# Performance work log

Hardware: AMD Instinct MI355X
Metric: run time of the kernel (lower is better)

The kernel has to match this reference:

```python
import jax, jax.numpy as jnp
import numpy as np

A, N, D, H, L, V = 2048, 64, 256, 8, 2, 119
DH = D // H


def _ln(x, g, b, eps=1e-5):
    m = x.mean(-1, keepdims=True)
    v = ((x - m) ** 2).mean(-1, keepdims=True)
    return (x - m) * jax.lax.rsqrt(v + eps) * g + b


def setup_inputs() -> dict:
    key = jax.random.key(0)
    ks = iter(jax.random.split(key, 64))
    nk = lambda: next(ks)
    inp = {
        'species': jax.random.randint(nk(), (A,), 0, V),
        'neighbor_species': jax.random.randint(nk(), (A, N), 0, V),
        'edge_vectors': jax.random.normal(nk(), (A, N, 3), jnp.float32),
        'edge_distances': jax.random.uniform(nk(), (A, N), jnp.float32) * 4.5,
        'padding_mask': jnp.zeros((A, N), bool),
        'reverse_neighbor_index': jax.random.randint(nk(), (A * N,), 0, A * N),
        'cutoff_factors': jax.random.uniform(nk(), (A, N), jnp.float32),
    }
    s = 0.05
    p = {
        'node_embed': jax.random.normal(nk(), (L, V, D), jnp.float32) * s,
        'neigh_embed': jax.random.normal(nk(), (V, D), jnp.float32) * s,
        'W_edge': jax.random.normal(nk(), (L, 4, D), jnp.float32) * s,
        'b_edge': jnp.zeros((L, D), jnp.float32),
        'ln1_g': jnp.ones((L, D), jnp.float32), 'ln1_b': jnp.zeros((L, D), jnp.float32),
        'Wqkv': jax.random.normal(nk(), (L, D, 3 * D), jnp.float32) * s,
        'bqkv': jnp.zeros((L, 3 * D), jnp.float32),
        'Wo': jax.random.normal(nk(), (L, D, D), jnp.float32) * s,
        'bo': jnp.zeros((L, D), jnp.float32),
        'ln2_g': jnp.ones((L, D), jnp.float32), 'ln2_b': jnp.zeros((L, D), jnp.float32),
        'Wff1': jax.random.normal(nk(), (L, D, 4 * D), jnp.float32) * s,
        'bff1': jnp.zeros((L, 4 * D), jnp.float32),
        'Wff2': jax.random.normal(nk(), (L, 4 * D, D), jnp.float32) * s,
        'bff2': jnp.zeros((L, D), jnp.float32),
        'Wnode': jax.random.normal(nk(), (L, D, D), jnp.float32) * s,
        'bnode': jnp.zeros((L, D), jnp.float32),
        'Wnh': jax.random.normal(nk(), (L, D, D), jnp.float32) * s,
        'bnh': jnp.zeros((L, D), jnp.float32),
        'Wnf': jax.random.normal(nk(), (L, D, 1), jnp.float32) * s,
        'bnf': jnp.zeros((L, 1), jnp.float32),
        'Weh': jax.random.normal(nk(), (L, D, D), jnp.float32) * s,
        'beh': jnp.zeros((L, D), jnp.float32),
        'Wef': jax.random.normal(nk(), (L, D, 1), jnp.float32) * s,
        'bef': jnp.zeros((L, 1), jnp.float32),
    }
    inp.update(p)
    return inp


def reference(species, neighbor_species, edge_vectors, edge_distances, padding_mask,
              reverse_neighbor_index, cutoff_factors, node_embed, neigh_embed,
              W_edge, b_edge, ln1_g, ln1_b, Wqkv, bqkv, Wo, bo, ln2_g, ln2_b,
              Wff1, bff1, Wff2, bff2, Wnode, bnode, Wnh, bnh, Wnf, bnf,
              Weh, beh, Wef, bef):
    inv = 1.0 / jnp.sqrt(jnp.asarray(DH, edge_vectors.dtype))
    mask = padding_mask  # [A,N] True = padded
    valid = (~mask).astype(edge_vectors.dtype)
    msgs = neigh_embed[neighbor_species]  # [A,N,D] gather (irregular)
    energies = jnp.zeros((A,), edge_vectors.dtype)
    for l in range(L):
        nodes = node_embed[l][species]  # [A,D]
        efeat = jnp.concatenate([edge_vectors, edge_distances[..., None]], -1)  # [A,N,4]
        eemb = jax.nn.gelu(efeat @ W_edge[l] + b_edge[l])
        x = msgs + eemb + nodes[:, None, :]  # [A,N,D] tokens
        # --- neighbor attention, modulated by cutoff envelope ---
        h = _ln(x, ln1_g[l], ln1_b[l])
        qkv = h @ Wqkv[l] + bqkv[l]
        q, k, v = jnp.split(qkv, 3, axis=-1)
        q = q.reshape(A, N, H, DH); k = k.reshape(A, N, H, DH); v = v.reshape(A, N, H, DH)
        scores = jnp.einsum('aihd,ajhd->ahij', q, k) * inv  # [A,H,N,N]
        scores = jnp.where(mask[:, None, None, :], -1e9, scores)
        probs = jax.nn.softmax(scores, axis=-1) * cutoff_factors[:, None, None, :]
        attn = jnp.einsum('ahij,ajhd->aihd', probs, v).reshape(A, N, D)
        x = x + attn @ Wo[l] + bo[l]
        h2 = _ln(x, ln2_g[l], ln2_b[l])
        x = x + jax.nn.gelu(h2 @ Wff1[l] + bff1[l]) @ Wff2[l] + bff2[l]
        output_edge = jnp.where(mask[..., None], 0.0, x)  # [A,N,D]
        pooled = (output_edge * (cutoff_factors * valid)[..., None]).sum(1)
        output_node = nodes + pooled @ Wnode[l] + bnode[l]
        # --- per-layer energy heads ---
        node_e = jax.nn.gelu(output_node @ Wnh[l] + bnh[l]) @ Wnf[l] + bnf[l]  # [A,1]
        edge_e = jax.nn.gelu(output_edge @ Weh[l] + beh[l]) @ Wef[l] + bef[l]  # [A,N,1]
        edge_e = jnp.where(mask[..., None], 0.0, edge_e)
        energies = energies + node_e[:, 0] + (edge_e[..., 0] * cutoff_factors).sum(1)
        # --- reverse-message scatter/gather mixing ---
        rev = output_edge.reshape(A * N, D)[reverse_neighbor_index].reshape(A, N, D)
        rev = jnp.where(mask[..., None], 0.0, rev)
        msgs = 0.5 * (msgs + rev)
    return energies
```

## Files before the change

### kernel.cpp

```cpp
#include <hip/hip_runtime.h>
#include <cstdint>


constexpr int A_ = 2048, N_ = 64, D_ = 256, H_ = 8, L_ = 2, V_ = 119;
constexpr int AN_ = A_ * N_;

typedef unsigned short bf16;
typedef __attribute__((ext_vector_type(4))) unsigned short u16x4;
typedef __attribute__((ext_vector_type(8))) short s16x8;
typedef __attribute__((ext_vector_type(4))) float f32x4;

__device__ __forceinline__ float bf2f(bf16 u) { return __uint_as_float((unsigned)u << 16); }
__device__ __forceinline__ bf16 f2bf(float f) {
  unsigned u = __float_as_uint(f);
  return (bf16)((u + 0x7fffu + ((u >> 16) & 1u)) >> 16);
}
__device__ __forceinline__ float4 ld4(const float* p) { return *(const float4*)p; }
__device__ __forceinline__ float4 ld4(const bf16* p) {
  u16x4 u = *(const u16x4*)p;
  return make_float4(bf2f(u.x), bf2f(u.y), bf2f(u.z), bf2f(u.w));
}
__device__ __forceinline__ void st4(float* p, float4 v) { *(float4*)p = v; }
__device__ __forceinline__ void st4(bf16* p, float4 v) {
  u16x4 u;
  u.x = f2bf(v.x); u.y = f2bf(v.y); u.z = f2bf(v.z); u.w = f2bf(v.w);
  *(u16x4*)p = u;
}
__device__ __forceinline__ float lds1(const float* p) { return *p; }
__device__ __forceinline__ float lds1(const bf16* p) { return bf2f(*p); }
__device__ __forceinline__ void sts1(float* p, float v) { *p = v; }
__device__ __forceinline__ void sts1(bf16* p, float v) { *p = f2bf(v); }

__device__ __forceinline__ float gelu_f(float x) {
  float z2 = 1.5957691216057308f * x * (1.f + 0.044715f * x * x);
  float e = __expf(-z2);
  return x * __builtin_amdgcn_rcpf(1.f + e);
}

__device__ __forceinline__ float wave_sum(float s) {
#pragma unroll
  for (int off = 32; off > 0; off >>= 1) s += __shfl_down(s, off, 64);
  return __shfl(s, 0, 64);
}

__device__ __forceinline__ void gload_lds16(const bf16* g, void* lds) {
  __builtin_amdgcn_global_load_lds(
      (const __attribute__((address_space(1))) unsigned int*)g,
      (__attribute__((address_space(3))) unsigned int*)lds, 16, 0, 0);
}

__global__ void zero_kernel(float* p, int n) {
  int i = blockIdx.x * 256 + threadIdx.x;
  if (i < n) p[i] = 0.f;
}

__global__ __launch_bounds__(256) void wt_kernel(
    const float* __restrict__ W, bf16* __restrict__ Wt, int K, int N) {
  int idx = blockIdx.x * 256 + threadIdx.x;
  if (idx >= K * N) return;
  int k = idx / N, n = idx - k * N;
  Wt[(size_t)n * K + k] = f2bf(W[idx]);
}

__global__ __launch_bounds__(256) void init_msgs_kernel(
    const int* __restrict__ ns, const float* __restrict__ ne, bf16* __restrict__ msgs) {
  int t = blockIdx.x, d = threadIdx.x;
  msgs[(size_t)t * D_ + d] = f2bf(ne[(size_t)ns[t] * D_ + d]);
}

__global__ __launch_bounds__(256) void gather_nodes_kernel(
    const int* __restrict__ species, const float* __restrict__ node_embed_l,
    float* __restrict__ nodesbuf) {
  int a = blockIdx.x, d = threadIdx.x;
  nodesbuf[(size_t)a * D_ + d] = node_embed_l[(size_t)species[a] * D_ + d];
}

__global__ __launch_bounds__(256) void build_x_ln_kernel(
    const bf16* __restrict__ msgs, const float* __restrict__ ev,
    const float* __restrict__ ed, const float* __restrict__ We,
    const float* __restrict__ be, const float* __restrict__ nodesbuf,
    const float* __restrict__ lng, const float* __restrict__ lnb,
    bf16* __restrict__ x, bf16* __restrict__ h, int token0) {
  int lt = blockIdx.x * 4 + (threadIdx.x >> 6);
  int t = token0 + lt;
  int lane = threadIdx.x & 63;
  int d4 = lane << 2;
  int a = t >> 6;
  float e0 = ev[(size_t)t * 3 + 0];
  float e1 = ev[(size_t)t * 3 + 1];
  float e2 = ev[(size_t)t * 3 + 2];
  float dd = ed[t];
  float4 m = ld4(msgs + (size_t)t * D_ + d4);
  float4 nb = ld4(nodesbuf + (size_t)a * D_ + d4);
  float4 w0 = ld4(We + d4);
  float4 w1 = ld4(We + D_ + d4);
  float4 w2 = ld4(We + 2 * D_ + d4);
  float4 w3 = ld4(We + 3 * D_ + d4);
  float4 bb = ld4(be + d4);
  float r[4];
  {
    float mm[4] = {m.x, m.y, m.z, m.w};
    float nn[4] = {nb.x, nb.y, nb.z, nb.w};
    float ww0[4] = {w0.x, w0.y, w0.z, w0.w};
    float ww1[4] = {w1.x, w1.y, w1.z, w1.w};
    float ww2[4] = {w2.x, w2.y, w2.z, w2.w};
    float ww3[4] = {w3.x, w3.y, w3.z, w3.w};
    float bbv[4] = {bb.x, bb.y, bb.z, bb.w};
#pragma unroll
    for (int c = 0; c < 4; ++c) {
      float tt = e0 * ww0[c] + e1 * ww1[c] + e2 * ww2[c] + dd * ww3[c] + bbv[c];
      r[c] = mm[c] + gelu_f(tt) + nn[c];
    }
  }
  st4(x + (size_t)lt * D_ + d4, make_float4(r[0], r[1], r[2], r[3]));
  float s = wave_sum(r[0] + r[1] + r[2] + r[3]);
  float mean = s * (1.f / 256.f);
  float c0 = r[0] - mean, c1 = r[1] - mean, c2 = r[2] - mean, c3 = r[3] - mean;
  float q = wave_sum(c0 * c0 + c1 * c1 + c2 * c2 + c3 * c3);
  float rstd = rsqrtf(q * (1.f / 256.f) + 1e-5f);
  float4 g4 = *(const float4*)(lng + d4);
  float4 b4 = *(const float4*)(lnb + d4);
  float4 o;
  o.x = c0 * rstd * g4.x + b4.x;
  o.y = c1 * rstd * g4.y + b4.y;
  o.z = c2 * rstd * g4.z + b4.z;
  o.w = c3 * rstd * g4.w + b4.w;
  st4(h + (size_t)lt * D_ + d4, o);
}

__global__ __launch_bounds__(256) void ln_apply_kernel(
    const bf16* __restrict__ x, const float* __restrict__ gw,
    const float* __restrict__ bw, bf16* __restrict__ h) {
  int row = blockIdx.x * 4 + (threadIdx.x >> 6);
  int lane = threadIdx.x & 63;
  float4 v = ld4(x + (size_t)row * D_ + lane * 4);
  float s = wave_sum(v.x + v.y + v.z + v.w);
  float mean = s * (1.f / 256.f);
  float dx = v.x - mean, dy = v.y - mean, dz = v.z - mean, dw = v.w - mean;
  float q = wave_sum(dx * dx + dy * dy + dz * dz + dw * dw);
  float rstd = rsqrtf(q * (1.f / 256.f) + 1e-5f);
  float4 g4 = *(const float4*)(gw + lane * 4);
  float4 b4 = *(const float4*)(bw + lane * 4);
  float4 o;
  o.x = dx * rstd * g4.x + b4.x;
  o.y = dy * rstd * g4.y + b4.y;
  o.z = dz * rstd * g4.z + b4.z;
  o.w = dw * rstd * g4.w + b4.w;
  st4(h + (size_t)row * D_ + lane * 4, o);
}

template <bool GELU, bool RES, typename TC>
__global__ __launch_bounds__(256) void mfma_gemm_kernel(
    const bf16* __restrict__ A, const bf16* __restrict__ Bt,
    const float* __restrict__ bias, const TC* __restrict__ Rp, TC* __restrict__ Cp,
    int M, int N, int K) {
  __shared__ __align__(16) char AlsB[128 * 64];
  __shared__ __align__(16) char BlsB[128 * 64];
  const int nb = N >> 7;
  const int bx = blockIdx.x % nb;
  const int by = blockIdx.x / nb;
  const int tid = threadIdx.x;
  const int w = tid >> 6, l = tid & 63;
  const int wm = w >> 1, wn = w & 1;
  const int srow = l >> 2;
  const int kg = (l & 3) ^ ((l >> 3) & 3);
  const bf16* Ag = A + (size_t)(by * 128 + w * 32 + srow) * K + kg * 8;
  const bf16* Bg = Bt + (size_t)(bx * 128 + w * 32 + srow) * K + kg * 8;
  char* AlsW = AlsB + w * 2048;
  char* BlsW = BlsB + w * 2048;
  const int frow = l & 15;
  const int soff = (((l >> 4) ^ ((l >> 1) & 3)) << 4);
  const char* Ar = AlsB + (wm * 64 + frow) * 64 + soff;
  const char* Br = BlsB + (wn * 64 + frow) * 64 + soff;

  f32x4 acc[4][4] = {};
  for (int k0 = 0; k0 < K; k0 += 32) {
    __syncthreads();
    gload_lds16(Ag + k0, AlsW);
    gload_lds16(Ag + (size_t)16 * K + k0, AlsW + 1024);
    gload_lds16(Bg + k0, BlsW);
    gload_lds16(Bg + (size_t)16 * K + k0, BlsW + 1024);
    __syncthreads();
    s16x8 af[4], bfr[4];
#pragma unroll
    for (int mi = 0; mi < 4; ++mi) af[mi] = *(const s16x8*)(Ar + mi * 1024);
#pragma unroll
    for (int nj = 0; nj < 4; ++nj) bfr[nj] = *(const s16x8*)(Br + nj * 1024);
#pragma unroll
    for (int mi = 0; mi < 4; ++mi)
#pragma unroll
      for (int nj = 0; nj < 4; ++nj)
        acc[mi][nj] = __builtin_amdgcn_mfma_f32_16x16x32_bf16(af[mi], bfr[nj],
                                                              acc[mi][nj], 0, 0, 0);
  }
  const int r0 = (l >> 4) << 2;
#pragma unroll
  for (int mi = 0; mi < 4; ++mi) {
    int rowb = by * 128 + wm * 64 + mi * 16 + r0;
#pragma unroll
    for (int r = 0; r < 4; ++r) {
      size_t rowoff = (size_t)(rowb + r) * N;
#pragma unroll
      for (int nj = 0; nj < 4; ++nj) {
        int col = bx * 128 + wn * 64 + nj * 16 + frow;
        float v = acc[mi][nj][r] + bias[col];
        if constexpr (GELU) v = gelu_f(v);
        if constexpr (RES) v += lds1(Rp + rowoff + col);
        sts1(Cp + rowoff + col, v);
      }
    }
  }
}

__global__ __launch_bounds__(256) void edge_head_kernel(
    const bf16* __restrict__ A, const bf16* __restrict__ Bt,
    const float* __restrict__ bias, const float* __restrict__ wef,
    float* __restrict__ edge_e, int M, int N, int K) {
  __shared__ __align__(16) char AlsB[128 * 64];
  __shared__ __align__(16) char BlsB[128 * 64];
  const int nb = N >> 7;
  const int bx = blockIdx.x % nb;
  const int by = blockIdx.x / nb;
  const int tid = threadIdx.x;
  const int w = tid >> 6, l = tid & 63;
  const int wm = w >> 1, wn = w & 1;
  const int srow = l >> 2;
  const int kg = (l & 3) ^ ((l >> 3) & 3);
  const bf16* Ag = A + (size_t)(by * 128 + w * 32 + srow) * K + kg * 8;
  const bf16* Bg = Bt + (size_t)(bx * 128 + w * 32 + srow) * K + kg * 8;
  char* AlsW = AlsB + w * 2048;
  char* BlsW = BlsB + w * 2048;
  const int frow = l & 15;
  const int soff = (((l >> 4) ^ ((l >> 1) & 3)) << 4);
  const char* Ar = AlsB + (wm * 64 + frow) * 64 + soff;
  const char* Br = BlsB + (wn * 64 + frow) * 64 + soff;

  f32x4 acc[4][4] = {};
  for (int k0 = 0; k0 < K; k0 += 32) {
    __syncthreads();
    gload_lds16(Ag + k0, AlsW);
    gload_lds16(Ag + (size_t)16 * K + k0, AlsW + 1024);
    gload_lds16(Bg + k0, BlsW);
    gload_lds16(Bg + (size_t)16 * K + k0, BlsW + 1024);
    __syncthreads();
    s16x8 af[4], bfr[4];
#pragma unroll
    for (int mi = 0; mi < 4; ++mi) af[mi] = *(const s16x8*)(Ar + mi * 1024);
#pragma unroll
    for (int nj = 0; nj < 4; ++nj) bfr[nj] = *(const s16x8*)(Br + nj * 1024);
#pragma unroll
    for (int mi = 0; mi < 4; ++mi)
#pragma unroll
      for (int nj = 0; nj < 4; ++nj)
        acc[mi][nj] = __builtin_amdgcn_mfma_f32_16x16x32_bf16(af[mi], bfr[nj],
                                                              acc[mi][nj], 0, 0, 0);
  }
  const int r0 = (l >> 4) << 2;
#pragma unroll
  for (int mi = 0; mi < 4; ++mi) {
#pragma unroll
    for (int r = 0; r < 4; ++r) {
      float s = 0.f;
#pragma unroll
      for (int nj = 0; nj < 4; ++nj) {
        int col = bx * 128 + wn * 64 + nj * 16 + frow;
        s += gelu_f(acc[mi][nj][r] + bias[col]) * wef[col];
      }
      s += __shfl_xor(s, 1, 64);
      s += __shfl_xor(s, 2, 64);
      s += __shfl_xor(s, 4, 64);
      s += __shfl_xor(s, 8, 64);
      if (frow == 0) {
        int row = by * 128 + wm * 64 + mi * 16 + r0 + r;
        atomicAdd(&edge_e[row], s);
      }
    }
  }
}

template <bool GELU, bool RES>
__global__ __launch_bounds__(256) void vgemm_kernel(
    const float* __restrict__ Ap, const float* __restrict__ Bp,
    const float* __restrict__ bias, const float* __restrict__ Rp,
    float* __restrict__ Cp, int M, int N, int K) {
  __shared__ float As[16][65];
  __shared__ float Bs[16][65];
  int nb = N >> 6;
  int bx = blockIdx.x % nb;
  int by = blockIdx.x / nb;
  int tid = threadIdx.x;
  int tx = tid & 15, ty = tid >> 4;
  int am = tid >> 2, akq = (tid & 3) << 2;
  int bk = tid >> 4, bc = (tid & 15) << 2;
  const float* Ab = Ap + (size_t)(by * 64) * K;
  const float* Bb = Bp + bx * 64;
  float acc[4][4] = {};
  for (int k0 = 0; k0 < K; k0 += 16) {
    float4 av = ld4(Ab + (size_t)am * K + k0 + akq);
    As[akq + 0][am] = av.x; As[akq + 1][am] = av.y;
    As[akq + 2][am] = av.z; As[akq + 3][am] = av.w;
    float4 bv4 = ld4(Bb + (size_t)(k0 + bk) * N + bc);
    Bs[bk][bc + 0] = bv4.x; Bs[bk][bc + 1] = bv4.y;
    Bs[bk][bc + 2] = bv4.z; Bs[bk][bc + 3] = bv4.w;
    __syncthreads();
#pragma unroll
    for (int k = 0; k < 16; ++k) {
      float ar[4], br[4];
#pragma unroll
      for (int i = 0; i < 4; ++i) ar[i] = As[k][ty * 4 + i];
#pragma unroll
      for (int j = 0; j < 4; ++j) br[j] = Bs[k][tx * 4 + j];
#pragma unroll
      for (int i = 0; i < 4; ++i)
#pragma unroll
        for (int j = 0; j < 4; ++j) acc[i][j] += ar[i] * br[j];
    }
    __syncthreads();
  }
#pragma unroll
  for (int i = 0; i < 4; ++i) {
    int row = by * 64 + ty * 4 + i;
    int col0 = bx * 64 + tx * 4;
    float4 v = make_float4(acc[i][0], acc[i][1], acc[i][2], acc[i][3]);
    float4 bs = *(const float4*)(bias + col0);
    v.x += bs.x; v.y += bs.y; v.z += bs.z; v.w += bs.w;
    if constexpr (GELU) {
      v.x = gelu_f(v.x); v.y = gelu_f(v.y); v.z = gelu_f(v.z); v.w = gelu_f(v.w);
    }
    if constexpr (RES) {
      float4 r = ld4(Rp + (size_t)row * N + col0);
      v.x += r.x; v.y += r.y; v.z += r.z; v.w += r.w;
    }
    st4(Cp + (size_t)row * N + col0, v);
  }
}

__global__ __launch_bounds__(64) void attn_kernel(
    const bf16* __restrict__ qkv, const float* __restrict__ cutoff,
    const unsigned char* __restrict__ mask, bf16* __restrict__ out, int atom0) {
  int al = blockIdx.x >> 3;
  int h = blockIdx.x & 7;
  int a = atom0 + al;
  int lane = threadIdx.x;
  __shared__ __align__(16) char Pl[64 * 128];
  __shared__ __align__(16) char Vt[32 * 128];
  const bf16* base = qkv + (size_t)al * (64 * 768);
  const int fr = lane & 15;
  const int kg8 = (lane >> 4) << 3;
  const int r0 = (lane >> 4) << 2;
  s16x8 qf[4], kf[4];
#pragma unroll
  for (int mi = 0; mi < 4; ++mi)
    qf[mi] = *(const s16x8*)(base + (size_t)(mi * 16 + fr) * 768 + h * 32 + kg8);
#pragma unroll
  for (int nj = 0; nj < 4; ++nj)
    kf[nj] = *(const s16x8*)(base + (size_t)(nj * 16 + fr) * 768 + 256 + h * 32 + kg8);
  {
    int vrow = lane >> 3;
    int d4 = (lane & 7) << 2;
#pragma unroll
    for (int it = 0; it < 8; ++it) {
      int row = it * 8 + vrow;
      u16x4 v = *(const u16x4*)(base + (size_t)row * 768 + 512 + h * 32 + d4);
#pragma unroll
      for (int c = 0; c < 4; ++c) {
        int d = d4 + c;
        int byt = (d * 128 + row * 2) ^ ((d & 7) << 4);
        *(bf16*)(Vt + byt) = v[c];
      }
    }
  }
  f32x4 s[4][4];
#pragma unroll
  for (int mi = 0; mi < 4; ++mi)
#pragma unroll
    for (int nj = 0; nj < 4; ++nj) {
      f32x4 z = {0.f, 0.f, 0.f, 0.f};
      s[mi][nj] = __builtin_amdgcn_mfma_f32_16x16x32_bf16(qf[mi], kf[nj], z, 0, 0, 0);
    }
  const float inv = 0.17677669529663687f;
  float cwj[4], mskj[4];
#pragma unroll
  for (int nj = 0; nj < 4; ++nj) {
    int j = nj * 16 + fr;
    cwj[nj] = cutoff[(size_t)a * 64 + j];
    mskj[nj] = mask[(size_t)a * 64 + j] ? 1.f : 0.f;
  }
  float rden[4][4];
#pragma unroll
  for (int mi = 0; mi < 4; ++mi) {
    float rm[4] = {-3e38f, -3e38f, -3e38f, -3e38f};
#pragma unroll
    for (int nj = 0; nj < 4; ++nj)
#pragma unroll
      for (int r = 0; r < 4; ++r) {
        float v = s[mi][nj][r] * inv;
        if (mskj[nj] != 0.f) v = -1e9f;
        s[mi][nj][r] = v;
        rm[r] = fmaxf(rm[r], v);
      }
#pragma unroll
    for (int r = 0; r < 4; ++r) {
      rm[r] = fmaxf(rm[r], __shfl_xor(rm[r], 1, 64));
      rm[r] = fmaxf(rm[r], __shfl_xor(rm[r], 2, 64));
      rm[r] = fmaxf(rm[r], __shfl_xor(rm[r], 4, 64));
      rm[r] = fmaxf(rm[r], __shfl_xor(rm[r], 8, 64));
    }
    float dn[4] = {0.f, 0.f, 0.f, 0.f};
#pragma unroll
    for (int nj = 0; nj < 4; ++nj)
#pragma unroll
      for (int r = 0; r < 4; ++r) {
        float e = __expf(s[mi][nj][r] - rm[r]);
        s[mi][nj][r] = e;
        dn[r] += e;
      }
#pragma unroll
    for (int r = 0; r < 4; ++r) {
      dn[r] += __shfl_xor(dn[r], 1, 64);
      dn[r] += __shfl_xor(dn[r], 2, 64);
      dn[r] += __shfl_xor(dn[r], 4, 64);
      dn[r] += __shfl_xor(dn[r], 8, 64);
      rden[mi][r] = dn[r];
    }
#pragma unroll
    for (int nj = 0; nj < 4; ++nj)
#pragma unroll
      for (int r = 0; r < 4; ++r) {
        int row = mi * 16 + r0 + r;
        int byt = (row * 128 + (nj * 16 + fr) * 2) ^ ((row & 7) << 4);
        *(bf16*)(Pl + byt) = f2bf(s[mi][nj][r] * cwj[nj]);
      }
  }
  __syncthreads();
  s16x8 bfv[2][2];
#pragma unroll
  for (int dj = 0; dj < 2; ++dj)
#pragma unroll
    for (int kk = 0; kk < 2; ++kk) {
      int d = dj * 16 + fr;
      int byt = (d * 128 + (kk * 32 + kg8) * 2) ^ ((d & 7) << 4);
      bfv[dj][kk] = *(const s16x8*)(Vt + byt);
    }
  f32x4 o[4][2] = {};
#pragma unroll
  for (int mi = 0; mi < 4; ++mi) {
#pragma unroll
    for (int kk = 0; kk < 2; ++kk) {
      int row = mi * 16 + fr;
      int byt = (row * 128 + (kk * 32 + kg8) * 2) ^ ((row & 7) << 4);
      s16x8 af = *(const s16x8*)(Pl + byt);
#pragma unroll
      for (int dj = 0; dj < 2; ++dj)
        o[mi][dj] = __builtin_amdgcn_mfma_f32_16x16x32_bf16(af, bfv[dj][kk],
                                                            o[mi][dj], 0, 0, 0);
    }
  }
#pragma unroll
  for (int mi = 0; mi < 4; ++mi) {
#pragma unroll
    for (int r = 0; r < 4; ++r) {
      float scr = __builtin_amdgcn_rcpf(rden[mi][r]);
      int row = mi * 16 + r0 + r;
      bf16* orow = out + (size_t)(al * 64 + row) * D_ + h * 32;
#pragma unroll
      for (int dj = 0; dj < 2; ++dj)
        orow[dj * 16 + fr] = f2bf(o[mi][dj][r] * scr);
    }
  }
}

__global__ __launch_bounds__(256) void pooled_kernel(
    const bf16* __restrict__ x, const float* __restrict__ cutoff,
    const unsigned char* __restrict__ mask, float* __restrict__ p0) {
  int a = blockIdx.x, d = threadIdx.x;
  __shared__ float w[64];
  if (d < 64) {
    int t = a * 64 + d;
    w[d] = mask[t] ? 0.f : cutoff[t];
  }
  __syncthreads();
  float acc = 0.f;
  const bf16* xb = x + (size_t)a * 64 * D_ + d;
#pragma unroll 8
  for (int n = 0; n < 64; ++n) acc += bf2f(xb[(size_t)n * D_]) * w[n];
  p0[(size_t)a * D_ + d] = acc;
}

template <typename TA>
__global__ __launch_bounds__(256) void rowdot_kernel(
    const TA* __restrict__ Ap, const float* __restrict__ w,
    const float* __restrict__ biasp, const unsigned char* __restrict__ mask,
    float* __restrict__ outp) {
  int row = blockIdx.x * 4 + (threadIdx.x >> 6);
  int lane = threadIdx.x & 63;
  float4 v = ld4(Ap + (size_t)row * D_ + lane * 4);
  float4 ww = *(const float4*)(w + lane * 4);
  float s = wave_sum(v.x * ww.x + v.y * ww.y + v.z * ww.z + v.w * ww.w);
  if (lane == 0) {
    float e = s + biasp[0];
    if (mask && mask[row]) e = 0.f;
    outp[row] = e;
  }
}

__global__ __launch_bounds__(64) void accum_energy_kernel(
    const float* __restrict__ node_e, const float* __restrict__ edge_e,
    const float* __restrict__ befp, const unsigned char* __restrict__ mask,
    const float* __restrict__ cutoff, float* __restrict__ energies) {
  int a = blockIdx.x, n = threadIdx.x;
  int t = a * 64 + n;
  float e = mask[t] ? 0.f : (edge_e[t] + befp[0]);
  float s = wave_sum(e * cutoff[t]);
  if (n == 0) energies[a] += node_e[a] + s;
}

__global__ __launch_bounds__(256) void rev_mix_kernel(
    const bf16* __restrict__ x, const int* __restrict__ rev,
    const unsigned char* __restrict__ mask, bf16* __restrict__ msgs) {
  size_t tid = (size_t)blockIdx.x * 256 + threadIdx.x;
  int token = int(tid >> 6);
  int d4 = int(tid & 63) << 2;
  int src = rev[token];
  float4 r = make_float4(0.f, 0.f, 0.f, 0.f);
  if (!mask[token] && !mask[src]) r = ld4(x + (size_t)src * D_ + d4);
  float4 m = ld4(msgs + (size_t)token * D_ + d4);
  m.x = 0.5f * (m.x + r.x);
  m.y = 0.5f * (m.y + r.y);
  m.z = 0.5f * (m.z + r.z);
  m.w = 0.5f * (m.w + r.w);
  st4(msgs + (size_t)token * D_ + d4, m);
}

extern "C" void kernel_launch(void* const* d_in, const int* in_sizes, int n_in,
                              void* d_out, int out_size, void* d_ws, size_t ws_size,
                              hipStream_t stream) {
  const int* species = (const int*)d_in[0];
  const int* nspecies = (const int*)d_in[1];
  const float* ev = (const float*)d_in[2];
  const float* ed = (const float*)d_in[3];
  const unsigned char* mask = (const unsigned char*)d_in[4];
  const int* rev = (const int*)d_in[5];
  const float* cutoff = (const float*)d_in[6];
  const float* node_embed = (const float*)d_in[7];
  const float* neigh_embed = (const float*)d_in[8];
  const float* W_edge = (const float*)d_in[9];
  const float* b_edge = (const float*)d_in[10];
  const float* ln1_g = (const float*)d_in[11];
  const float* ln1_b = (const float*)d_in[12];
  const float* Wqkv = (const float*)d_in[13];
  const float* bqkv = (const float*)d_in[14];
  const float* Wo = (const float*)d_in[15];
  const float* bo = (const float*)d_in[16];
  const float* ln2_g = (const float*)d_in[17];
  const float* ln2_b = (const float*)d_in[18];
  const float* Wff1 = (const float*)d_in[19];
  const float* bff1 = (const float*)d_in[20];
  const float* Wff2 = (const float*)d_in[21];
  const float* bff2 = (const float*)d_in[22];
  const float* Wnode = (const float*)d_in[23];
  const float* bnode = (const float*)d_in[24];
  const float* Wnh = (const float*)d_in[25];
  const float* bnh = (const float*)d_in[26];
  const float* Wnf = (const float*)d_in[27];
  const float* bnf = (const float*)d_in[28];
  const float* Weh = (const float*)d_in[29];
  const float* beh = (const float*)d_in[30];
  const float* Wef = (const float*)d_in[31];
  const float* bef = (const float*)d_in[32];
  float* out = (float*)d_out;

  int CHv = 8;
  if (ws_size >= (size_t)330000000) CHv = 2;
  else if (ws_size >= (size_t)240000000) CHv = 4;
  const int RW = AN_ / CHv;
  const int ATC = A_ / CHv;

  char* wsb = (char*)d_ws;
  size_t off = 0;
  auto alloc = [&](size_t bytes) {
    void* p = wsb + off;
    off += (bytes + 255) & ~(size_t)255;
    return p;
  };
  bf16* msgs = (bf16*)alloc((size_t)AN_ * D_ * 2);
  bf16* x = (bf16*)alloc((size_t)AN_ * D_ * 2);
  bf16* U1 = (bf16*)alloc((size_t)RW * D_ * 2);
  bf16* U2 = (bf16*)alloc((size_t)RW * 1024 * 2);
  bf16* WqkvT = (bf16*)alloc((size_t)L_ * 768 * 256 * 2);
  bf16* WoT = (bf16*)alloc((size_t)L_ * 256 * 256 * 2);
  bf16* Wff1T = (bf16*)alloc((size_t)L_ * 1024 * 256 * 2);
  bf16* Wff2T = (bf16*)alloc((size_t)L_ * 256 * 1024 * 2);
  bf16* WehT = (bf16*)alloc((size_t)L_ * 256 * 256 * 2);
  float* nodesbuf = (float*)alloc((size_t)A_ * D_ * 4);
  float* node_e = (float*)alloc((size_t)A_ * 4);
  float* edge_e = (float*)alloc((size_t)AN_ * 4);
  float* p0 = (float*)U2;
  float* p1 = p0 + (size_t)A_ * D_;
  float* p2 = p1 + (size_t)A_ * D_;
  (void)in_sizes; (void)n_in; (void)out_size;

  for (int l = 0; l < L_; ++l) {
    wt_kernel<<<(256 * 768 + 255) / 256, 256, 0, stream>>>(
        Wqkv + (size_t)l * 256 * 768, WqkvT + (size_t)l * 768 * 256, 256, 768);
    wt_kernel<<<(256 * 256 + 255) / 256, 256, 0, stream>>>(
        Wo + (size_t)l * 256 * 256, WoT + (size_t)l * 256 * 256, 256, 256);
    wt_kernel<<<(256 * 1024 + 255) / 256, 256, 0, stream>>>(
        Wff1 + (size_t)l * 256 * 1024, Wff1T + (size_t)l * 1024 * 256, 256, 1024);
    wt_kernel<<<(1024 * 256 + 255) / 256, 256, 0, stream>>>(
        Wff2 + (size_t)l * 1024 * 256, Wff2T + (size_t)l * 256 * 1024, 1024, 256);
    wt_kernel<<<(256 * 256 + 255) / 256, 256, 0, stream>>>(
        Weh + (size_t)l * 256 * 256, WehT + (size_t)l * 256 * 256, 256, 256);
  }

  zero_kernel<<<(A_ + 255) / 256, 256, 0, stream>>>(out, A_);
  init_msgs_kernel<<<AN_, 256, 0, stream>>>(nspecies, neigh_embed, msgs);

  for (int l = 0; l < L_; ++l) {
    gather_nodes_kernel<<<A_, 256, 0, stream>>>(
        species, node_embed + (size_t)l * V_ * D_, nodesbuf);
    for (int c = 0; c < CHv; ++c) {
      bf16* xc = x + (size_t)c * RW * D_;
      build_x_ln_kernel<<<RW / 4, 256, 0, stream>>>(
          msgs, ev, ed, W_edge + (size_t)l * 4 * D_, b_edge + (size_t)l * D_,
          nodesbuf, ln1_g + (size_t)l * D_, ln1_b + (size_t)l * D_,
          xc, U1, c * RW);
      mfma_gemm_kernel<false, false, bf16><<<(RW / 128) * (768 / 128), 256, 0, stream>>>(
          U1, WqkvT + (size_t)l * 768 * 256, bqkv + (size_t)l * 768, (const bf16*)nullptr,
          U2, RW, 768, 256);
      attn_kernel<<<ATC * H_, 64, 0, stream>>>(U2, cutoff, mask, U1, c * ATC);
      mfma_gemm_kernel<false, true, bf16><<<(RW / 128) * (256 / 128), 256, 0, stream>>>(
          U1, WoT + (size_t)l * 256 * 256, bo + (size_t)l * D_, xc, xc, RW, 256, 256);
    }
    for (int c = 0; c < CHv; ++c) {
      bf16* xc = x + (size_t)c * RW * D_;
      ln_apply_kernel<<<RW / 4, 256, 0, stream>>>(
          xc, ln2_g + (size_t)l * D_, ln2_b + (size_t)l * D_, U1);
      mfma_gemm_kernel<true, false, bf16><<<(RW / 128) * (1024 / 128), 256, 0, stream>>>(
          U1, Wff1T + (size_t)l * 1024 * 256, bff1 + (size_t)l * 1024, (const bf16*)nullptr,
          U2, RW, 1024, 256);
      mfma_gemm_kernel<false, true, bf16><<<(RW / 128) * (256 / 128), 256, 0, stream>>>(
          U2, Wff2T + (size_t)l * 256 * 1024, bff2 + (size_t)l * D_, xc, xc,
          RW, 256, 1024);
    }
    pooled_kernel<<<A_, 256, 0, stream>>>(x, cutoff, mask, p0);
    vgemm_kernel<false, true><<<(A_ / 64) * (256 / 64), 256, 0, stream>>>(
        p0, Wnode + (size_t)l * D_ * D_, bnode + (size_t)l * D_, nodesbuf, p1,
        A_, 256, 256);
    vgemm_kernel<true, false><<<(A_ / 64) * (256 / 64), 256, 0, stream>>>(
        p1, Wnh + (size_t)l * D_ * D_, bnh + (size_t)l * D_, nullptr, p2, A_, 256, 256);
    rowdot_kernel<float><<<A_ / 4, 256, 0, stream>>>(
        p2, Wnf + (size_t)l * D_, bnf + l, nullptr, node_e);
    zero_kernel<<<(AN_ + 255) / 256, 256, 0, stream>>>(edge_e, AN_);
    edge_head_kernel<<<(AN_ / 128) * (256 / 128), 256, 0, stream>>>(
        x, WehT + (size_t)l * 256 * 256, beh + (size_t)l * D_, Wef + (size_t)l * D_,
        edge_e, AN_, 256, 256);
    accum_energy_kernel<<<A_, 64, 0, stream>>>(node_e, edge_e, bef + l, mask, cutoff, out);
    rev_mix_kernel<<<AN_ * 64 / 256, 256, 0, stream>>>(x, rev, mask, msgs);
  }
}
```

Before: 1.923 ms.

## Fuse feed-forward GEMMs into one kernel keeping the hidden activation in LDS

```diff
diff --git a/kernel.cpp b/kernel.cpp
--- a/kernel.cpp
+++ b/kernel.cpp
@@ -210,6 +210,98 @@
       }
     }
   }
+}
+
+__global__ __launch_bounds__(256) void ff_fused_kernel(
+    const bf16* __restrict__ h, const bf16* __restrict__ W1t,
+    const float* __restrict__ b1, const bf16* __restrict__ W2t,
+    const float* __restrict__ b2, bf16* __restrict__ xio) {
+  __shared__ __align__(16) char Hl[64 * 512];
+  __shared__ __align__(16) char Tl[64 * 256];
+  const int tid = threadIdx.x;
+  const int wv = tid >> 6, l = tid & 63;
+  const int fr = l & 15;
+  const int kg8 = (l >> 4) << 3;
+  const int r0 = (l >> 4) << 2;
+  const size_t row0 = (size_t)blockIdx.x * 64;
+#pragma unroll
+  for (int p = 0; p < 8; ++p) {
+    int offs = p * 4096 + wv * 1024;
+    int row = (offs >> 9) + (l >> 5);
+    int gs = (l & 31) ^ (row & 7);
+    gload_lds16(h + (row0 + row) * 256 + gs * 8, Hl + offs);
+  }
+  __syncthreads();
+
+  f32x4 accO[4][4] = {};
+  for (int hb = 0; hb < 8; ++hb) {
+    f32x4 accT[4][2] = {};
+#pragma unroll
+    for (int ks = 0; ks < 8; ++ks) {
+      int kb = (ks * 32 + kg8) * 2;
+      s16x8 af[4];
+#pragma unroll
+      for (int mi = 0; mi < 4; ++mi) {
+        int hr = mi * 16 + fr;
+        af[mi] = *(const s16x8*)(Hl + ((hr * 512 + kb) ^ ((hr & 7) << 4)));
+      }
+#pragma unroll
+      for (int nj = 0; nj < 2; ++nj) {
+        int col1 = hb * 128 + wv * 32 + nj * 16 + fr;
+        s16x8 bw = *(const s16x8*)(W1t + (size_t)col1 * 256 + ks * 32 + kg8);
+#pragma unroll
+        for (int mi = 0; mi < 4; ++mi)
+          accT[mi][nj] = __builtin_amdgcn_mfma_f32_16x16x32_bf16(af[mi], bw,
+                                                                 accT[mi][nj], 0, 0, 0);
+      }
+    }
+    if (hb) __syncthreads();
+#pragma unroll
+    for (int nj = 0; nj < 2; ++nj) {
+      int tcol = wv * 32 + nj * 16 + fr;
+      float b1v = b1[hb * 128 + tcol];
+#pragma unroll
+      for (int mi = 0; mi < 4; ++mi)
+#pragma unroll
+        for (int rr = 0; rr < 4; ++rr) {
+          int trow = mi * 16 + r0 + rr;
+          int byt = (trow * 256 + tcol * 2) ^ ((trow & 7) << 4);
+          *(bf16*)(Tl + byt) = f2bf(gelu_f(accT[mi][nj][rr] + b1v));
+        }
+    }
+    __syncthreads();
+#pragma unroll
+    for (int kk = 0; kk < 4; ++kk) {
+      int kb = (kk * 32 + kg8) * 2;
+      s16x8 paf[4];
+#pragma unroll
+      for (int mi = 0; mi < 4; ++mi) {
+        int tr = mi * 16 + fr;
+        paf[mi] = *(const s16x8*)(Tl + ((tr * 256 + kb) ^ ((tr & 7) << 4)));
+      }
+#pragma unroll
+      for (int nj = 0; nj < 4; ++nj) {
+        int col2 = wv * 64 + nj * 16 + fr;
+        s16x8 bw = *(const s16x8*)(W2t + (size_t)col2 * 1024 + hb * 128 + kk * 32 + kg8);
+#pragma unroll
+        for (int mi = 0; mi < 4; ++mi)
+          accO[mi][nj] = __builtin_amdgcn_mfma_f32_16x16x32_bf16(paf[mi], bw,
+                                                                 accO[mi][nj], 0, 0, 0);
+      }
+    }
+  }
+#pragma unroll
+  for (int mi = 0; mi < 4; ++mi)
+#pragma unroll
+    for (int rr = 0; rr < 4; ++rr) {
+      size_t row = row0 + mi * 16 + r0 + rr;
+#pragma unroll
+      for (int nj = 0; nj < 4; ++nj) {
+        int col = wv * 64 + nj * 16 + fr;
+        float v = accO[mi][nj][rr] + b2[col] + bf2f(xio[row * 256 + col]);
+        xio[row * 256 + col] = f2bf(v);
+      }
+    }
 }
 
 __global__ __launch_bounds__(256) void edge_head_kernel(
@@ -575,6 +667,8 @@
   else if (ws_size >= (size_t)240000000) CHv = 4;
   const int RW = AN_ / CHv;
   const int ATC = A_ / CHv;
+  const int CHf = (CHv >= 8) ? 2 : 1;
+  const int RWf = AN_ / CHf;
 
   char* wsb = (char*)d_ws;
   size_t off = 0;
@@ -632,16 +726,13 @@
       mfma_gemm_kernel<false, true, bf16><<<(RW / 128) * (256 / 128), 256, 0, stream>>>(
           U1, WoT + (size_t)l * 256 * 256, bo + (size_t)l * D_, xc, xc, RW, 256, 256);
     }
-    for (int c = 0; c < CHv; ++c) {
-      bf16* xc = x + (size_t)c * RW * D_;
-      ln_apply_kernel<<<RW / 4, 256, 0, stream>>>(
-          xc, ln2_g + (size_t)l * D_, ln2_b + (size_t)l * D_, U1);
-      mfma_gemm_kernel<true, false, bf16><<<(RW / 128) * (1024 / 128), 256, 0, stream>>>(
-          U1, Wff1T + (size_t)l * 1024 * 256, bff1 + (size_t)l * 1024, (const bf16*)nullptr,
-          U2, RW, 1024, 256);
-      mfma_gemm_kernel<false, true, bf16><<<(RW / 128) * (256 / 128), 256, 0, stream>>>(
-          U2, Wff2T + (size_t)l * 256 * 1024, bff2 + (size_t)l * D_, xc, xc,
-          RW, 256, 1024);
+    for (int cf = 0; cf < CHf; ++cf) {
+      bf16* xc = x + (size_t)cf * RWf * D_;
+      ln_apply_kernel<<<RWf / 4, 256, 0, stream>>>(
+          xc, ln2_g + (size_t)l * D_, ln2_b + (size_t)l * D_, U2);
+      ff_fused_kernel<<<RWf / 64, 256, 0, stream>>>(
+          U2, Wff1T + (size_t)l * 1024 * 256, bff1 + (size_t)l * 1024,
+          Wff2T + (size_t)l * 256 * 1024, bff2 + (size_t)l * D_, xc);
     }
     pooled_kernel<<<A_, 256, 0, stream>>>(x, cutoff, mask, p0);
     vgemm_kernel<false, true><<<(A_ / 64) * (256 / 64), 256, 0, stream>>>(
```

New measurement: 2.031 ms. 1.06x slower.
